# Kernel tuning notes

Hardware: AMD Instinct MI355X
Metric: run time of the kernel (lower is better)

Reference implementation:

```python
import math
import jax, jax.numpy as jnp
import numpy as np

B, T, D, H, FACTOR = 8, 4096, 1024, 16, 5
DH = D // H


def setup_inputs() -> dict:
    key = jax.random.key(0)
    ks = jax.random.split(key, 7)
    u = max(1, min(int(FACTOR * math.log(T + 1)), T))  # = 41
    s = 1.0 / np.sqrt(D).astype(np.float32)
    x = jax.random.normal(ks[0], (B, T, D), jnp.float32)
    Wq = jax.random.normal(ks[1], (D, D), jnp.float32) * s
    Wk = jax.random.normal(ks[2], (D, D), jnp.float32) * s
    Wv = jax.random.normal(ks[3], (D, D), jnp.float32) * s
    Wo = jax.random.normal(ks[4], (D, D), jnp.float32) * s
    bo = jax.random.normal(ks[5], (D,), jnp.float32) * 0.01
    # unique indices, mirroring torch.randperm(T)[:u]
    idx = jax.random.permutation(ks[6], T)[:u].astype(jnp.int32)
    return {"x": x, "Wq": Wq, "Wk": Wk, "Wv": Wv, "Wo": Wo, "bo": bo, "idx": idx}


def reference(x, Wq, Wk, Wv, Wo, bo, idx):
    Bx, Tx, Dx = x.shape
    scale = 1.0 / np.sqrt(DH).astype(np.float32)

    def proj(W):  # torch Linear: x @ W.T, then split heads -> [B,H,T,Dh]
        return (x @ W.T).reshape(Bx, Tx, H, DH).transpose(0, 2, 1, 3)

    Q = proj(Wq)
    K = proj(Wk)
    V = proj(Wv)

    Qs = Q[:, :, idx, :]                                   # [B,H,u,Dh] gather
    scores = jnp.einsum('bhud,bhtd->bhut', Qs, K) * scale  # [B,H,u,T]
    attn = jax.nn.softmax(scores, axis=-1)
    ctx = jnp.einsum('bhut,bhtd->bhud', attn, V)           # [B,H,u,Dh]

    # mean over the u sampled positions fills non-sampled slots
    out = jnp.broadcast_to(ctx.mean(axis=2, keepdims=True), (Bx, H, Tx, DH))
    out = out.at[:, :, idx, :].set(ctx)                    # scatter ctx back

    y = out.transpose(0, 2, 1, 3).reshape(Bx, Tx, Dx)
    return y @ Wo.T + bo
```

## Files before the change

kernel.cpp:

```cpp
#include <hip/hip_runtime.h>
#include <hip/hip_bf16.h>

#define B_  8
#define T_  4096
#define D_  1024
#define H_  16
#define DH_ 64
#define NC_ 4

typedef __bf16 bf8 __attribute__((ext_vector_type(8)));
typedef float f32x4 __attribute__((ext_vector_type(4)));

__device__ __forceinline__ unsigned short f2bf_rn(float f) {
    unsigned u = __float_as_uint(f);
    unsigned r = (u + 0x7FFF + ((u >> 16) & 1)) >> 16;
    return (unsigned short)r;
}

__device__ __forceinline__ void async_load16(const void* gp, void* lp) {
    __builtin_amdgcn_global_load_lds(
        (const __attribute__((address_space(1))) unsigned*)(gp),
        (__attribute__((address_space(3))) unsigned*)(lp), 16, 0, 0);
}


__global__ void k_sel(const int* __restrict__ idx, int* __restrict__ sel, int U) {
    for (int t = threadIdx.x; t < T_; t += 256) sel[t] = 0;
    __syncthreads();
    if (threadIdx.x < U) sel[idx[threadIdx.x]] = threadIdx.x + 1;
}

__global__ void k_gather(const float* __restrict__ x, const int* __restrict__ idx,
                         float* __restrict__ xs, int U) {
    int bi = blockIdx.x;
    int b = bi / U, i = bi - b * U;
    int t = idx[i];
    const float4* src = (const float4*)(x + ((size_t)(b * T_ + t)) * D_);
    float4* dst = (float4*)(xs + (size_t)bi * D_);
    dst[threadIdx.x] = src[threadIdx.x];
}

__global__ void k_cvt_flat(const float* __restrict__ src, short* __restrict__ dst) {
    size_t i = ((size_t)blockIdx.x * 256 + threadIdx.x) * 8;
    float4 a = *(const float4*)(src + i);
    float4 b = *(const float4*)(src + i + 4);
    short4 s0, s1;
    s0.x = (short)f2bf_rn(a.x); s0.y = (short)f2bf_rn(a.y);
    s0.z = (short)f2bf_rn(a.z); s0.w = (short)f2bf_rn(a.w);
    s1.x = (short)f2bf_rn(b.x); s1.y = (short)f2bf_rn(b.y);
    s1.z = (short)f2bf_rn(b.z); s1.w = (short)f2bf_rn(b.w);
    *(short4*)(dst + i) = s0;
    *(short4*)(dst + i + 4) = s1;
}

__global__ void k_zpad(short* __restrict__ Qtb, int HU, int MP) {
    int bi = blockIdx.x;
    int npad = MP - HU;
    int b = bi / npad, r = bi - b * npad;
    short4 z = {0, 0, 0, 0};
    *(short4*)(Qtb + ((size_t)b * MP + HU + r) * D_ + threadIdx.x * 4) = z;
}

__global__ __launch_bounds__(256) void k_proj(const float* __restrict__ A,
                                              const float* __restrict__ W,
                                              const float* __restrict__ bias,
                                              float* __restrict__ C, int M) {
    __shared__ float As[32][64 + 4];
    __shared__ float Bs[32][64 + 4];
    int m0 = blockIdx.x * 64, n0 = blockIdx.y * 64;
    int tid = threadIdx.x;
    int lr = tid >> 3;
    int lc = (tid & 7) * 4;
    int ty = tid >> 4, tx = tid & 15;
    float acc[4][4] = {{0.f}};
    for (int k0 = 0; k0 < D_; k0 += 32) {
#pragma unroll
        for (int half = 0; half < 2; ++half) {
            int r = lr + half * 32;
            int gm = m0 + r;
            float4 v = make_float4(0.f, 0.f, 0.f, 0.f);
            if (gm < M) v = *(const float4*)(A + (size_t)gm * D_ + k0 + lc);
            As[lc + 0][r] = v.x; As[lc + 1][r] = v.y; As[lc + 2][r] = v.z; As[lc + 3][r] = v.w;
            int gn = n0 + r;
            float4 w = *(const float4*)(W + (size_t)gn * D_ + k0 + lc);
            Bs[lc + 0][r] = w.x; Bs[lc + 1][r] = w.y; Bs[lc + 2][r] = w.z; Bs[lc + 3][r] = w.w;
        }
        __syncthreads();
#pragma unroll
        for (int kk = 0; kk < 32; ++kk) {
            float4 a = *(const float4*)&As[kk][ty * 4];
            float4 bb = *(const float4*)&Bs[kk][tx * 4];
            acc[0][0] += a.x * bb.x; acc[0][1] += a.x * bb.y; acc[0][2] += a.x * bb.z; acc[0][3] += a.x * bb.w;
            acc[1][0] += a.y * bb.x; acc[1][1] += a.y * bb.y; acc[1][2] += a.y * bb.z; acc[1][3] += a.y * bb.w;
            acc[2][0] += a.z * bb.x; acc[2][1] += a.z * bb.y; acc[2][2] += a.z * bb.z; acc[2][3] += a.z * bb.w;
            acc[3][0] += a.w * bb.x; acc[3][1] += a.w * bb.y; acc[3][2] += a.w * bb.z; acc[3][3] += a.w * bb.w;
        }
        __syncthreads();
    }
#pragma unroll
    for (int i = 0; i < 4; ++i) {
        int gm = m0 + ty * 4 + i;
        if (gm < M) {
            int gn = n0 + tx * 4;
            float4 v = make_float4(acc[i][0], acc[i][1], acc[i][2], acc[i][3]);
            if (bias) {
                v.x += bias[gn + 0]; v.y += bias[gn + 1];
                v.z += bias[gn + 2]; v.w += bias[gn + 3];
            }
            *(float4*)(C + (size_t)gm * D_ + gn) = v;
        }
    }
}

__global__ __launch_bounds__(256) void k_qth(const float* __restrict__ Qs,
                                             const float* __restrict__ Wk,
                                             short* __restrict__ Qtb, int U, int MP) {
    __shared__ float As[32][64 + 4];
    __shared__ float Bs[32][64 + 4];
    int h = blockIdx.z;
    int m0 = blockIdx.x * 64, n0 = blockIdx.y * 64;
    int BU = B_ * U;
    int tid = threadIdx.x;
    int lr = tid >> 3, lc = (tid & 7) * 4;
    int ty = tid >> 4, tx = tid & 15;
    float acc[4][4] = {{0.f}};
    for (int k0 = 0; k0 < DH_; k0 += 32) {
#pragma unroll
        for (int half = 0; half < 2; ++half) {
            int r = lr + half * 32;
            int gm = m0 + r;
            float4 v = make_float4(0.f, 0.f, 0.f, 0.f);
            if (gm < BU) v = *(const float4*)(Qs + (size_t)gm * D_ + h * DH_ + k0 + lc);
            As[lc + 0][r] = v.x; As[lc + 1][r] = v.y; As[lc + 2][r] = v.z; As[lc + 3][r] = v.w;
            int kr = (tid >> 4) + half * 16;
            int nc = (tid & 15) * 4;
            float4 w = *(const float4*)(Wk + ((size_t)(h * DH_ + k0 + kr)) * D_ + n0 + nc);
            *(float4*)&Bs[kr][nc] = w;
        }
        __syncthreads();
#pragma unroll
        for (int kk = 0; kk < 32; ++kk) {
            float4 a = *(const float4*)&As[kk][ty * 4];
            float4 bb = *(const float4*)&Bs[kk][tx * 4];
            acc[0][0] += a.x * bb.x; acc[0][1] += a.x * bb.y; acc[0][2] += a.x * bb.z; acc[0][3] += a.x * bb.w;
            acc[1][0] += a.y * bb.x; acc[1][1] += a.y * bb.y; acc[1][2] += a.y * bb.z; acc[1][3] += a.y * bb.w;
            acc[2][0] += a.z * bb.x; acc[2][1] += a.z * bb.y; acc[2][2] += a.z * bb.z; acc[2][3] += a.z * bb.w;
            acc[3][0] += a.w * bb.x; acc[3][1] += a.w * bb.y; acc[3][2] += a.w * bb.z; acc[3][3] += a.w * bb.w;
        }
        __syncthreads();
    }
#pragma unroll
    for (int i = 0; i < 4; ++i) {
        int gm = m0 + ty * 4 + i;
        if (gm < BU) {
            int b = gm / U, ii = gm - b * U;
            short4 s;
            s.x = (short)f2bf_rn(0.125f * acc[i][0]);
            s.y = (short)f2bf_rn(0.125f * acc[i][1]);
            s.z = (short)f2bf_rn(0.125f * acc[i][2]);
            s.w = (short)f2bf_rn(0.125f * acc[i][3]);
            *(short4*)(Qtb + ((size_t)b * MP + h * U + ii) * D_ + n0 + tx * 4) = s;
        }
    }
}

__global__ __launch_bounds__(256) void k_scores_exp(const short* __restrict__ A,
                                                    const short* __restrict__ Bt,
                                                    short* __restrict__ attnb, int MP) {
    __shared__ short As[128 * 32];
    __shared__ short Bs[128 * 32];
    int g = blockIdx.x;
    int n8 = (g >> 3) & 3;
    int m = (g >> 5) % 6;
    int b = (g >> 5) / 6;
    int n = (g & 7) + 8 * n8;
    const int K = D_;
    const short* Ab = A + (size_t)b * MP * K;
    const short* Bb = Bt + (size_t)b * T_ * K;
    short* Cb = attnb + (size_t)b * MP * T_;
    int m0 = m * 128, n0 = n * 128;
    int tid = threadIdx.x;
    int lane = tid & 63, w = tid >> 6;
    int wr = w >> 1, wc = w & 1;

    f32x4 acc[4][4];
#pragma unroll
    for (int mi = 0; mi < 4; ++mi)
#pragma unroll
        for (int ni = 0; ni < 4; ++ni)
            acc[mi][ni] = (f32x4){0.f, 0.f, 0.f, 0.f};

    int arow = wr * 64 + (lane & 15);
    int brow = wc * 64 + (lane & 15);
    int koff = (lane >> 4) * 8;

    for (int kt = 0; kt < K; kt += 32) {
#pragma unroll
        for (int i = 0; i < 2; ++i) {
            int li = i * 256 + tid;
            int row = li >> 2, kc = (li & 3) << 3;
            async_load16(Ab + (size_t)(m0 + row) * K + kt + kc, As + li * 8);
            async_load16(Bb + (size_t)(n0 + row) * K + kt + kc, Bs + li * 8);
        }
        __syncthreads();
        bf8 af[4], bfr[4];
#pragma unroll
        for (int mi = 0; mi < 4; ++mi)
            af[mi] = *(const bf8*)(As + (arow + mi * 16) * 32 + koff);
#pragma unroll
        for (int ni = 0; ni < 4; ++ni)
            bfr[ni] = *(const bf8*)(Bs + (brow + ni * 16) * 32 + koff);
#pragma unroll
        for (int mi = 0; mi < 4; ++mi)
#pragma unroll
            for (int ni = 0; ni < 4; ++ni)
                acc[mi][ni] = __builtin_amdgcn_mfma_f32_16x16x32_bf16(af[mi], bfr[ni], acc[mi][ni], 0, 0, 0);
        __syncthreads();
    }

    int cr = (lane >> 4) * 4, cc = lane & 15;
#pragma unroll
    for (int mi = 0; mi < 4; ++mi)
#pragma unroll
        for (int ni = 0; ni < 4; ++ni) {
            int col = n0 + wc * 64 + ni * 16 + cc;
#pragma unroll
            for (int r = 0; r < 4; ++r) {
                float e = __expf(acc[mi][ni][r]);
                int grow = m0 + wr * 64 + mi * 16 + cr + r;
                Cb[(size_t)grow * T_ + col] = (short)f2bf_rn(e);
            }
        }
}

__global__ __launch_bounds__(256) void k_v(const short* __restrict__ xb,
                                           const short* __restrict__ Wvb,
                                           short* __restrict__ Vt) {
    __shared__ short smem[8192];
    short* As = smem;
    short* Bs = smem + 4096;
    int g = blockIdx.x;
    int mr = g & 7, n = (g >> 3) & 7, mq = g >> 6;
    int m = mq * 8 + mr;
    const int K = D_;
    const short* Ab = xb + (size_t)m * 128 * K;
    const short* Bb = Wvb + (size_t)n * 128 * K;
    int tid = threadIdx.x;
    int lane = tid & 63, w = tid >> 6;
    int wr = w >> 1, wc = w & 1;

    f32x4 acc[4][4];
#pragma unroll
    for (int mi = 0; mi < 4; ++mi)
#pragma unroll
        for (int ni = 0; ni < 4; ++ni)
            acc[mi][ni] = (f32x4){0.f, 0.f, 0.f, 0.f};

    int arow = wr * 64 + (lane & 15);
    int brow = wc * 64 + (lane & 15);
    int koff = (lane >> 4) * 8;

    for (int kt = 0; kt < K; kt += 32) {
#pragma unroll
        for (int i = 0; i < 2; ++i) {
            int li = i * 256 + tid;
            int row = li >> 2, kc = (li & 3) << 3;
            async_load16(Ab + (size_t)row * K + kt + kc, As + li * 8);
            async_load16(Bb + (size_t)row * K + kt + kc, Bs + li * 8);
        }
        __syncthreads();
        bf8 af[4], bfr[4];
#pragma unroll
        for (int mi = 0; mi < 4; ++mi)
            af[mi] = *(const bf8*)(As + (arow + mi * 16) * 32 + koff);
#pragma unroll
        for (int ni = 0; ni < 4; ++ni)
            bfr[ni] = *(const bf8*)(Bs + (brow + ni * 16) * 32 + koff);
#pragma unroll
        for (int mi = 0; mi < 4; ++mi)
#pragma unroll
            for (int ni = 0; ni < 4; ++ni)
                acc[mi][ni] = __builtin_amdgcn_mfma_f32_16x16x32_bf16(af[mi], bfr[ni], acc[mi][ni], 0, 0, 0);
        __syncthreads();
    }

    int b = m >> 5;
    int tG0 = (m & 31) * 128 + wr * 64;
    int h = n * 2 + wc;
    short* ep = smem + w * 2048;
    const int PITCH = 72;
    int quad = lane >> 4;
#pragma unroll
    for (int ni = 0; ni < 4; ++ni) {
#pragma unroll
        for (int mi = 0; mi < 4; ++mi) {
            int t = mi * 16 + quad * 4;
            int dh = lane & 15;
#pragma unroll
            for (int r = 0; r < 4; ++r)
                ep[dh * PITCH + t + r] = (short)f2bf_rn(acc[mi][ni][r]);
        }
        __syncthreads();
#pragma unroll
        for (int it = 0; it < 2; ++it) {
            int dhl = it * 8 + (lane >> 3);
            int seg = lane & 7;
            bf8 v = *(const bf8*)(ep + dhl * PITCH + seg * 8);
            int dh = ni * 16 + dhl;
            *(bf8*)(Vt + ((size_t)(b * H_ + h) * DH_ + dh) * T_ + tG0 + seg * 8) = v;
        }
        __syncthreads();
    }
}

__global__ __launch_bounds__(256) void k_pv(const short* __restrict__ attnb,
                                            const short* __restrict__ Vt,
                                            float* __restrict__ Op,
                                            float* __restrict__ rsp,
                                            int U, int MP) {
    __shared__ short vt[64 * 136];
    int gid = blockIdx.x;
    int c = gid & (NC_ - 1);
    int bh = gid >> 2;
    int h = bh & (H_ - 1);
    int b = bh >> 4;
    int tid = threadIdx.x;
    int lane = tid & 63, w = tid >> 6;
    int quad = lane >> 4;
    const short* Arow = attnb + ((size_t)b * MP + h * U) * T_;
    const short* Vrow = Vt + (size_t)bh * DH_ * T_;

    f32x4 O[3];
#pragma unroll
    for (int mi = 0; mi < 3; ++mi) O[mi] = (f32x4){0.f, 0.f, 0.f, 0.f};
    float rs[3] = {0.f, 0.f, 0.f};

    for (int tt = 0; tt < (T_ / NC_) / 128; ++tt) {
        int t0 = c * (T_ / NC_) + tt * 128;
#pragma unroll
        for (int it = 0; it < 4; ++it) {
            int idx = it * 256 + tid;
            int dh = idx >> 4, seg = idx & 15;
            bf8 v = *(const bf8*)(Vrow + (size_t)dh * T_ + t0 + seg * 8);
            *(bf8*)(vt + dh * 136 + seg * 8) = v;
        }
        __syncthreads();
        bf8 af[3][4];
#pragma unroll
        for (int mi = 0; mi < 3; ++mi)
#pragma unroll
            for (int kf = 0; kf < 4; ++kf)
                af[mi][kf] = *(const bf8*)(Arow + (size_t)(mi * 16 + (lane & 15)) * T_ + t0 + kf * 32 + quad * 8);
        if (w == 0) {
#pragma unroll
            for (int mi = 0; mi < 3; ++mi)
#pragma unroll
                for (int kf = 0; kf < 4; ++kf)
#pragma unroll
                    for (int j = 0; j < 8; ++j) rs[mi] += (float)af[mi][kf][j];
        }
#pragma unroll
        for (int kf = 0; kf < 4; ++kf) {
            bf8 bfr = *(const bf8*)(vt + (w * 16 + (lane & 15)) * 136 + kf * 32 + quad * 8);
#pragma unroll
            for (int mi = 0; mi < 3; ++mi)
                O[mi] = __builtin_amdgcn_mfma_f32_16x16x32_bf16(af[mi][kf], bfr, O[mi], 0, 0, 0);
        }
        __syncthreads();
    }
#pragma unroll
    for (int mi = 0; mi < 3; ++mi)
#pragma unroll
        for (int r = 0; r < 4; ++r)
            Op[((size_t)gid * 48 + mi * 16 + quad * 4 + r) * DH_ + w * 16 + (lane & 15)] = O[mi][r];
    if (w == 0) {
#pragma unroll
        for (int mi = 0; mi < 3; ++mi) {
            rs[mi] += __shfl_xor(rs[mi], 16);
            rs[mi] += __shfl_xor(rs[mi], 32);
            if (quad == 0) rsp[(size_t)gid * 48 + mi * 16 + lane] = rs[mi];
        }
    }
}

__global__ __launch_bounds__(256) void k_rows2(const float* __restrict__ Op,
                                               const float* __restrict__ rsp,
                                               float* __restrict__ R, int U) {
    __shared__ float inv[48];
    __shared__ float msum[4][64];
    int bh = blockIdx.x;
    int b = bh >> 4, h = bh & (H_ - 1);
    int tid = threadIdx.x;
    if (tid < 48) {
        float s = 0.f;
        for (int cc = 0; cc < NC_; ++cc) s += rsp[(size_t)(bh * NC_ + cc) * 48 + tid];
        inv[tid] = 1.f / s;
    }
    __syncthreads();
    int dh = tid & 63, ig = tid >> 6;
    float acc = 0.f;
    for (int p = 0; p < 11; ++p) {
        int i = p * 4 + ig;
        if (i < U) {
            float o = 0.f;
            for (int cc = 0; cc < NC_; ++cc)
                o += Op[((size_t)(bh * NC_ + cc) * 48 + i) * DH_ + dh];
            float v = o * inv[i];
            R[((size_t)b * (U + 1) + 1 + i) * D_ + h * DH_ + dh] = v;
            acc += v;
        }
    }
    msum[ig][dh] = acc;
    __syncthreads();
    if (ig == 0)
        R[((size_t)b * (U + 1)) * D_ + h * DH_ + dh] =
            (msum[0][dh] + msum[1][dh] + msum[2][dh] + msum[3][dh]) / (float)U;
}

__global__ __launch_bounds__(256) void k_fill(const float* __restrict__ Yr,
                                              const int* __restrict__ sel,
                                              float* __restrict__ y, int U) {
    int blk = blockIdx.x;
    int b = blk >> 12, t = blk & (T_ - 1);
    int j = sel[t];
    const float4* src = (const float4*)(Yr + ((size_t)b * (U + 1) + j) * D_);
    float4* dst = (float4*)(y + (size_t)blk * D_);
    dst[threadIdx.x] = src[threadIdx.x];
}

extern "C" void kernel_launch(void* const* d_in, const int* in_sizes, int n_in,
                              void* d_out, int out_size, void* d_ws, size_t ws_size,
                              hipStream_t stream) {
    const float* x  = (const float*)d_in[0];
    const float* Wq = (const float*)d_in[1];
    const float* Wk = (const float*)d_in[2];
    const float* Wv = (const float*)d_in[3];
    const float* Wo = (const float*)d_in[4];
    const float* bo = (const float*)d_in[5];
    const int*  idx = (const int*)d_in[6];
    int U = in_sizes[6];
    int HU = H_ * U;
    int MP = ((HU + 127) / 128) * 128;

    char* w = (char*)d_ws;
    auto alloc = [&](size_t bytes) { char* p = w; w += (bytes + 255) & ~(size_t)255; return p; };

    float* xs    = (float*)alloc((size_t)B_ * U * D_ * 4);
    float* Qs    = (float*)alloc((size_t)B_ * U * D_ * 4);
    short* Qtb   = (short*)alloc((size_t)B_ * MP * D_ * 2);
    short* xb    = (short*)alloc((size_t)B_ * T_ * D_ * 2);
    short* Wvb   = (short*)alloc((size_t)D_ * D_ * 2);
    short* attnb = (short*)alloc((size_t)B_ * MP * T_ * 2);
    short* Vtb   = (short*)alloc((size_t)B_ * D_ * T_ * 2);
    float* Opb   = (float*)alloc((size_t)B_ * H_ * NC_ * 48 * DH_ * 4);
    float* rspb  = (float*)alloc((size_t)B_ * H_ * NC_ * 48 * 4);
    float* R     = (float*)alloc((size_t)B_ * (U + 1) * D_ * 4);
    float* Yr    = (float*)alloc((size_t)B_ * (U + 1) * D_ * 4);
    int*   sel   = (int*)alloc((size_t)T_ * 4);

    k_sel<<<dim3(1), dim3(256), 0, stream>>>(idx, sel, U);
    k_gather<<<dim3(B_ * U), dim3(256), 0, stream>>>(x, idx, xs, U);
    k_proj<<<dim3((B_ * U + 63) / 64, D_ / 64), dim3(256), 0, stream>>>(xs, Wq, nullptr, Qs, B_ * U);
    k_cvt_flat<<<dim3((size_t)B_ * T_ * D_ / 2048), dim3(256), 0, stream>>>(x, xb);
    k_cvt_flat<<<dim3((size_t)D_ * D_ / 2048), dim3(256), 0, stream>>>(Wv, Wvb);
    k_zpad<<<dim3(B_ * (MP - HU)), dim3(256), 0, stream>>>(Qtb, HU, MP);
    k_qth<<<dim3((B_ * U + 63) / 64, D_ / 64, H_), dim3(256), 0, stream>>>(Qs, Wk, Qtb, U, MP);
    k_scores_exp<<<dim3(8 * 4 * 6 * B_), dim3(256), 0, stream>>>(Qtb, xb, attnb, MP);
    k_v<<<dim3(2048), dim3(256), 0, stream>>>(xb, Wvb, Vtb);
    k_pv<<<dim3(B_ * H_ * NC_), dim3(256), 0, stream>>>(attnb, Vtb, Opb, rspb, U, MP);
    k_rows2<<<dim3(B_ * H_), dim3(256), 0, stream>>>(Opb, rspb, R, U);
    k_proj<<<dim3((B_ * (U + 1) + 63) / 64, D_ / 64), dim3(256), 0, stream>>>(R, Wo, bo, Yr, B_ * (U + 1));
    k_fill<<<dim3(B_ * T_), dim3(256), 0, stream>>>(Yr, sel, (float*)d_out, U);
}
```

Measured before the change: 592.2 us.

## Rewrite scores and V GEMMs with 256x256 double-buffered swizzled tiles

```diff
diff --git a/kernel.cpp b/kernel.cpp
--- a/kernel.cpp
+++ b/kernel.cpp
@@ -164,150 +164,175 @@
     }
 }
 
-__global__ __launch_bounds__(256) void k_scores_exp(const short* __restrict__ A,
-                                                    const short* __restrict__ Bt,
-                                                    short* __restrict__ attnb, int MP) {
-    __shared__ short As[128 * 32];
-    __shared__ short Bs[128 * 32];
-    int g = blockIdx.x;
-    int n8 = (g >> 3) & 3;
-    int m = (g >> 5) % 6;
-    int b = (g >> 5) / 6;
-    int n = (g & 7) + 8 * n8;
-    const int K = D_;
-    const short* Ab = A + (size_t)b * MP * K;
-    const short* Bb = Bt + (size_t)b * T_ * K;
-    short* Cb = attnb + (size_t)b * MP * T_;
-    int m0 = m * 128, n0 = n * 128;
+#define GEMM_NT 16
+
+__device__ __forceinline__ void stage64(const short* __restrict__ Ag,
+                                        const short* __restrict__ Bg,
+                                        short* lA, short* lB, int kt, int tid) {
+#pragma unroll
+    for (int i = 0; i < 4; ++i) {
+        int li = i * 512 + tid;
+        int row = li >> 3, sl = li & 7;
+        int off = row * D_ + kt + ((sl ^ (row & 7)) << 3);
+        async_load16(Ag + off, lA + li * 8);
+        async_load16(Bg + off, lB + li * 8);
+    }
+}
+
+__device__ __forceinline__ bf8 lds_frag(const short* l, int R, int slot) {
+    return *(const bf8*)(l + R * 64 + (((slot) ^ (R & 7)) << 3));
+}
+
+__device__ __forceinline__ void gemm256_core(const short* __restrict__ Ag,
+                                             const short* __restrict__ Bg,
+                                             short* lA0, short* lB0,
+                                             f32x4 (&acc)[8][4]) {
     int tid = threadIdx.x;
     int lane = tid & 63, w = tid >> 6;
-    int wr = w >> 1, wc = w & 1;
-
-    f32x4 acc[4][4];
-#pragma unroll
-    for (int mi = 0; mi < 4; ++mi)
+    int wr = w >> 2, wc = w & 3;
+    int ln = lane & 15, q = lane >> 4;
+#pragma unroll
+    for (int mi = 0; mi < 8; ++mi)
 #pragma unroll
         for (int ni = 0; ni < 4; ++ni)
             acc[mi][ni] = (f32x4){0.f, 0.f, 0.f, 0.f};
 
-    int arow = wr * 64 + (lane & 15);
-    int brow = wc * 64 + (lane & 15);
-    int koff = (lane >> 4) * 8;
-
-    for (int kt = 0; kt < K; kt += 32) {
-#pragma unroll
-        for (int i = 0; i < 2; ++i) {
-            int li = i * 256 + tid;
-            int row = li >> 2, kc = (li & 3) << 3;
-            async_load16(Ab + (size_t)(m0 + row) * K + kt + kc, As + li * 8);
-            async_load16(Bb + (size_t)(n0 + row) * K + kt + kc, Bs + li * 8);
-        }
-        __syncthreads();
-        bf8 af[4], bfr[4];
+    stage64(Ag, Bg, lA0, lB0, 0, tid);
+    stage64(Ag, Bg, lA0 + 16384, lB0 + 16384, 64, tid);
+
+#pragma unroll 1
+    for (int t = 0; t < GEMM_NT; ++t) {
+        const int p = t & 1;
+        short* lA = lA0 + p * 16384;
+        short* lB = lB0 + p * 16384;
+        if (t < GEMM_NT - 1) asm volatile("s_waitcnt vmcnt(8)" ::: "memory");
+        else                 asm volatile("s_waitcnt vmcnt(0)" ::: "memory");
+        __builtin_amdgcn_s_barrier();
+
+        bf8 bfrag[4][2], afrag[4][2];
+#pragma unroll
+        for (int ni = 0; ni < 4; ++ni)
+#pragma unroll
+            for (int kh = 0; kh < 2; ++kh)
+                bfrag[ni][kh] = lds_frag(lB, wc * 64 + ni * 16 + ln, kh * 4 + q);
 #pragma unroll
         for (int mi = 0; mi < 4; ++mi)
-            af[mi] = *(const bf8*)(As + (arow + mi * 16) * 32 + koff);
-#pragma unroll
-        for (int ni = 0; ni < 4; ++ni)
-            bfr[ni] = *(const bf8*)(Bs + (brow + ni * 16) * 32 + koff);
+#pragma unroll
+            for (int kh = 0; kh < 2; ++kh)
+                afrag[mi][kh] = lds_frag(lA, wr * 128 + mi * 16 + ln, kh * 4 + q);
+        __builtin_amdgcn_s_setprio(1);
+#pragma unroll
+        for (int kh = 0; kh < 2; ++kh)
+#pragma unroll
+            for (int mi = 0; mi < 4; ++mi)
+#pragma unroll
+                for (int ni = 0; ni < 4; ++ni)
+                    acc[mi][ni] = __builtin_amdgcn_mfma_f32_16x16x32_bf16(
+                        afrag[mi][kh], bfrag[ni][kh], acc[mi][ni], 0, 0, 0);
+        __builtin_amdgcn_s_setprio(0);
 #pragma unroll
         for (int mi = 0; mi < 4; ++mi)
 #pragma unroll
-            for (int ni = 0; ni < 4; ++ni)
-                acc[mi][ni] = __builtin_amdgcn_mfma_f32_16x16x32_bf16(af[mi], bfr[ni], acc[mi][ni], 0, 0, 0);
-        __syncthreads();
-    }
-
-    int cr = (lane >> 4) * 4, cc = lane & 15;
-#pragma unroll
-    for (int mi = 0; mi < 4; ++mi)
+            for (int kh = 0; kh < 2; ++kh)
+                afrag[mi][kh] = lds_frag(lA, wr * 128 + 64 + mi * 16 + ln, kh * 4 + q);
+        __builtin_amdgcn_s_setprio(1);
+#pragma unroll
+        for (int kh = 0; kh < 2; ++kh)
+#pragma unroll
+            for (int mi = 0; mi < 4; ++mi)
+#pragma unroll
+                for (int ni = 0; ni < 4; ++ni)
+                    acc[4 + mi][ni] = __builtin_amdgcn_mfma_f32_16x16x32_bf16(
+                        afrag[mi][kh], bfrag[ni][kh], acc[4 + mi][ni], 0, 0, 0);
+        __builtin_amdgcn_s_setprio(0);
+        asm volatile("" ::: "memory");
+        __builtin_amdgcn_s_barrier();
+        if (t + 2 < GEMM_NT)
+            stage64(Ag, Bg, lA, lB, (t + 2) * 64, tid);
+    }
+}
+
+__global__ __launch_bounds__(512, 2) void k_scores2(const short* __restrict__ Qtb,
+                                                    const short* __restrict__ xb,
+                                                    short* __restrict__ attnb, int MP) {
+    __shared__ short lA[2][16384];
+    __shared__ short lB[2][16384];
+    int bid = blockIdx.x;
+    int lg = (bid & 7) * (gridDim.x >> 3) + (bid >> 3);
+    int MT = MP >> 8;
+    int per_b = MT << 4;
+    int b = lg / per_b;
+    int r = lg - b * per_b;
+    int mt = r >> 4, nt = r & 15;
+    const short* Ag = Qtb + ((size_t)b * MP + mt * 256) * D_;
+    const short* Bg = xb + ((size_t)b * T_ + nt * 256) * D_;
+    f32x4 acc[8][4];
+    gemm256_core(Ag, Bg, &lA[0][0], &lB[0][0], acc);
+
+    short* Cb = attnb + (size_t)b * MP * T_;
+    int tid = threadIdx.x;
+    int lane = tid & 63, w = tid >> 6;
+    int wr = w >> 2, wc = w & 3;
+    int ln = lane & 15, q = lane >> 4;
+    int row0 = mt * 256 + wr * 128;
+    int col0 = nt * 256 + wc * 64;
+#pragma unroll
+    for (int mi = 0; mi < 8; ++mi)
 #pragma unroll
         for (int ni = 0; ni < 4; ++ni) {
-            int col = n0 + wc * 64 + ni * 16 + cc;
-#pragma unroll
-            for (int r = 0; r < 4; ++r) {
-                float e = __expf(acc[mi][ni][r]);
-                int grow = m0 + wr * 64 + mi * 16 + cr + r;
-                Cb[(size_t)grow * T_ + col] = (short)f2bf_rn(e);
+            int col = col0 + ni * 16 + ln;
+#pragma unroll
+            for (int rr = 0; rr < 4; ++rr) {
+                int grow = row0 + mi * 16 + q * 4 + rr;
+                Cb[(size_t)grow * T_ + col] = (short)f2bf_rn(__expf(acc[mi][ni][rr]));
             }
         }
 }
 
-__global__ __launch_bounds__(256) void k_v(const short* __restrict__ xb,
-                                           const short* __restrict__ Wvb,
-                                           short* __restrict__ Vt) {
-    __shared__ short smem[8192];
-    short* As = smem;
-    short* Bs = smem + 4096;
-    int g = blockIdx.x;
-    int mr = g & 7, n = (g >> 3) & 7, mq = g >> 6;
-    int m = mq * 8 + mr;
-    const int K = D_;
-    const short* Ab = xb + (size_t)m * 128 * K;
-    const short* Bb = Wvb + (size_t)n * 128 * K;
+__global__ __launch_bounds__(512, 2) void k_v2(const short* __restrict__ xb,
+                                               const short* __restrict__ Wvb,
+                                               short* __restrict__ Vt) {
+    __shared__ short lA[2][16384];
+    __shared__ short lB[2][16384];
+    int bid = blockIdx.x;
+    int lg = (bid & 7) * (gridDim.x >> 3) + (bid >> 3);
+    int mt = lg >> 2, nt = lg & 3;
+    const short* Ag = xb + (size_t)mt * 256 * D_;
+    const short* Bg = Wvb + (size_t)nt * 256 * D_;
+    f32x4 acc[8][4];
+    gemm256_core(Ag, Bg, &lA[0][0], &lB[0][0], acc);
+
     int tid = threadIdx.x;
     int lane = tid & 63, w = tid >> 6;
-    int wr = w >> 1, wc = w & 1;
-
-    f32x4 acc[4][4];
-#pragma unroll
-    for (int mi = 0; mi < 4; ++mi)
-#pragma unroll
-        for (int ni = 0; ni < 4; ++ni)
-            acc[mi][ni] = (f32x4){0.f, 0.f, 0.f, 0.f};
-
-    int arow = wr * 64 + (lane & 15);
-    int brow = wc * 64 + (lane & 15);
-    int koff = (lane >> 4) * 8;
-
-    for (int kt = 0; kt < K; kt += 32) {
-#pragma unroll
-        for (int i = 0; i < 2; ++i) {
-            int li = i * 256 + tid;
-            int row = li >> 2, kc = (li & 3) << 3;
-            async_load16(Ab + (size_t)row * K + kt + kc, As + li * 8);
-            async_load16(Bb + (size_t)row * K + kt + kc, Bs + li * 8);
-        }
-        __syncthreads();
-        bf8 af[4], bfr[4];
-#pragma unroll
-        for (int mi = 0; mi < 4; ++mi)
-            af[mi] = *(const bf8*)(As + (arow + mi * 16) * 32 + koff);
-#pragma unroll
-        for (int ni = 0; ni < 4; ++ni)
-            bfr[ni] = *(const bf8*)(Bs + (brow + ni * 16) * 32 + koff);
-#pragma unroll
-        for (int mi = 0; mi < 4; ++mi)
-#pragma unroll
-            for (int ni = 0; ni < 4; ++ni)
-                acc[mi][ni] = __builtin_amdgcn_mfma_f32_16x16x32_bf16(af[mi], bfr[ni], acc[mi][ni], 0, 0, 0);
-        __syncthreads();
-    }
-
-    int b = m >> 5;
-    int tG0 = (m & 31) * 128 + wr * 64;
-    int h = n * 2 + wc;
-    short* ep = smem + w * 2048;
-    const int PITCH = 72;
-    int quad = lane >> 4;
+    int wr = w >> 2, wc = w & 3;
+    int ln = lane & 15, q = lane >> 4;
+    int h = nt * 4 + wc;
+    int b = mt >> 4;
+    int tIn = (mt & 15) * 256 + wr * 128;
+    const int PITCH = 136;
+    short* ep = &lA[0][0] + w * 2304;
+    size_t vbase = ((size_t)(b * H_ + h) * DH_) * T_;
 #pragma unroll
     for (int ni = 0; ni < 4; ++ni) {
 #pragma unroll
-        for (int mi = 0; mi < 4; ++mi) {
-            int t = mi * 16 + quad * 4;
-            int dh = lane & 15;
-#pragma unroll
-            for (int r = 0; r < 4; ++r)
-                ep[dh * PITCH + t + r] = (short)f2bf_rn(acc[mi][ni][r]);
+        for (int mi = 0; mi < 8; ++mi) {
+            short4 s;
+            s.x = (short)f2bf_rn(acc[mi][ni][0]);
+            s.y = (short)f2bf_rn(acc[mi][ni][1]);
+            s.z = (short)f2bf_rn(acc[mi][ni][2]);
+            s.w = (short)f2bf_rn(acc[mi][ni][3]);
+            *(short4*)(ep + ln * PITCH + mi * 16 + q * 4) = s;
         }
         __syncthreads();
 #pragma unroll
         for (int it = 0; it < 2; ++it) {
             int dhl = it * 8 + (lane >> 3);
             int seg = lane & 7;
-            bf8 v = *(const bf8*)(ep + dhl * PITCH + seg * 8);
+            bf8 v0 = *(const bf8*)(ep + dhl * PITCH + seg * 8);
+            bf8 v1 = *(const bf8*)(ep + dhl * PITCH + (seg + 8) * 8);
             int dh = ni * 16 + dhl;
-            *(bf8*)(Vt + ((size_t)(b * H_ + h) * DH_ + dh) * T_ + tG0 + seg * 8) = v;
+            *(bf8*)(Vt + vbase + (size_t)dh * T_ + tIn + seg * 8) = v0;
+            *(bf8*)(Vt + vbase + (size_t)dh * T_ + tIn + 64 + seg * 8) = v1;
         }
         __syncthreads();
     }
@@ -458,6 +483,8 @@
     float* Yr    = (float*)alloc((size_t)B_ * (U + 1) * D_ * 4);
     int*   sel   = (int*)alloc((size_t)T_ * 4);
 
+    int MT = MP / 256;
+
     k_sel<<<dim3(1), dim3(256), 0, stream>>>(idx, sel, U);
     k_gather<<<dim3(B_ * U), dim3(256), 0, stream>>>(x, idx, xs, U);
     k_proj<<<dim3((B_ * U + 63) / 64, D_ / 64), dim3(256), 0, stream>>>(xs, Wq, nullptr, Qs, B_ * U);
@@ -465,8 +492,8 @@
     k_cvt_flat<<<dim3((size_t)D_ * D_ / 2048), dim3(256), 0, stream>>>(Wv, Wvb);
     k_zpad<<<dim3(B_ * (MP - HU)), dim3(256), 0, stream>>>(Qtb, HU, MP);
     k_qth<<<dim3((B_ * U + 63) / 64, D_ / 64, H_), dim3(256), 0, stream>>>(Qs, Wk, Qtb, U, MP);
-    k_scores_exp<<<dim3(8 * 4 * 6 * B_), dim3(256), 0, stream>>>(Qtb, xb, attnb, MP);
-    k_v<<<dim3(2048), dim3(256), 0, stream>>>(xb, Wvb, Vtb);
+    k_scores2<<<dim3(B_ * MT * 16), dim3(512), 0, stream>>>(Qtb, xb, attnb, MP);
+    k_v2<<<dim3((B_ * T_ / 256) * (D_ / 256)), dim3(512), 0, stream>>>(xb, Wvb, Vtb);
     k_pv<<<dim3(B_ * H_ * NC_), dim3(256), 0, stream>>>(attnb, Vtb, Opb, rspb, U, MP);
     k_rows2<<<dim3(B_ * H_), dim3(256), 0, stream>>>(Opb, rspb, R, U);
     k_proj<<<dim3((B_ * (U + 1) + 63) / 64, D_ / 64), dim3(256), 0, stream>>>(R, Wo, bo, Yr, B_ * (U + 1));
```

After: 587.9 us. About the same (-0.7%).
